# Kernel optimization log

Measured on AMD Instinct MI355X. Metric: run time of the kernel, lower is better.

The kernel has to match this reference:

```python
import jax, jax.numpy as jnp
import numpy as np

E = 64          # num_experts
TOPK = 8        # num_experts_per_tok
I = 512         # moe_intermediate_size
H = 1024        # hidden_size
G = 128         # awq group_size
T = 2048        # tokens (batch*seq)

# AWQ nibble unpack order: bit shifts [0,16,4,20,8,24,12,28] -> indices [0,4,1,5,2,6,3,7]
_AWQ_SHIFTS = jnp.array([0, 4, 1, 5, 2, 6, 3, 7], dtype=jnp.int32) * 4


def awq_dequant(qw, qz, scales, group_size=G):
    """qw: (K, N//8) int32, qz: (K//G, N//8) int32, scales: (K//G, N) float.
    Returns dense weight (K, N): (q - z) * scale with per-group zero/scale."""
    K = qw.shape[0]
    uq = ((qw[:, :, None] >> _AWQ_SHIFTS) & 0xF).reshape(K, -1)          # (K, N)
    uz = ((qz[:, :, None] >> _AWQ_SHIFTS) & 0xF).reshape(qz.shape[0], -1)  # (K//G, N)
    uz = jnp.repeat(uz, group_size, axis=0)                               # (K, N)
    sc = jnp.repeat(scales, group_size, axis=0)                           # (K, N)
    return (uq.astype(scales.dtype) - uz.astype(scales.dtype)) * sc


def setup_inputs() -> dict:
    key = jax.random.key(0)
    ks = jax.random.split(key, 8)
    imax = 2**31 - 1
    return {
        "x": jax.random.normal(ks[0], (T, H), dtype=jnp.float32),
        "gate_w": jax.random.normal(ks[1], (E, H), dtype=jnp.float32) * 0.02,
        "qweight1": jax.random.randint(ks[2], (H, (E * I) // 8), 0, imax, dtype=jnp.int32),
        "qzeros1": jax.random.randint(ks[3], (H // G, (E * I) // 8), 0, imax, dtype=jnp.int32),
        "scales1": jax.random.normal(ks[4], (H // G, E * I), dtype=jnp.float32) * 0.02,
        "qweight2": jax.random.randint(ks[5], (I, (E * H) // 8), 0, imax, dtype=jnp.int32),
        "qzeros2": jax.random.randint(ks[6], (I // G, (E * H) // 8), 0, imax, dtype=jnp.int32),
        "scales2": jax.random.normal(ks[7], (I // G, E * H), dtype=jnp.float32) * 0.02,
    }


def reference(x, gate_w, qweight1, qzeros1, scales1, qweight2, qzeros2, scales2):
    # dequant grouped expert weights
    w1 = awq_dequant(qweight1, qzeros1, scales1).T.reshape(E, I, H)   # (E, I, H)
    w2 = awq_dequant(qweight2, qzeros2, scales2).T.reshape(E, H, I)   # (E, H, I)

    # routing: softmax -> top-k -> renormalize
    logits = x @ gate_w.T                                             # (T, E)
    probs = jax.nn.softmax(logits, axis=-1)
    topv, topi = jax.lax.top_k(probs, TOPK)                           # (T, K)
    topv = topv / jnp.sum(topv, axis=-1, keepdims=True)
    cw = jnp.sum(jax.nn.one_hot(topi, E, dtype=x.dtype) * topv[..., None], axis=1)  # (T, E)

    # experts: out = sum_e cw[t,e] * silu(x @ w1[e].T) @ w2[e].T
    h = jax.nn.silu(jnp.einsum('th,eih->tei', x, w1))                 # (T, E, I)
    h = h * cw[:, :, None]                                            # fold combine weights
    out = jnp.einsum('tei,ehi->th', h, w2)                            # (T, H)
    return out
```

## Files before the change

kernel.cpp:

```cpp
#include <hip/hip_runtime.h>
#include <hip/hip_bf16.h>

#define T_TOK 2048
#define HID   1024
#define EXP   64
#define TOPK  8
#define IMED  512
#define N1 (EXP * IMED)
#define C1 (N1 / 8)
#define N2 (EXP * HID)
#define C2 (N2 / 8)

typedef _Float16 h16x2 __attribute__((ext_vector_type(2)));
typedef _Float16 h16x8 __attribute__((ext_vector_type(8)));
typedef float f32x4 __attribute__((ext_vector_type(4)));
typedef unsigned short ushortx4 __attribute__((ext_vector_type(4)));
typedef unsigned short ushortx8 __attribute__((ext_vector_type(8)));

__constant__ int kShifts[8] = {0, 16, 4, 20, 8, 24, 12, 28};

__device__ __forceinline__ void async16(const void* g, void* l) {
  __builtin_amdgcn_global_load_lds((const __attribute__((address_space(1))) void*)g,
                                   (__attribute__((address_space(3))) void*)l, 16, 0, 0);
}

__device__ __forceinline__ unsigned short f2h(float f) {
  return __builtin_bit_cast(unsigned short, (_Float16)f);
}
__device__ __forceinline__ float h2f(unsigned short b) {
  return (float)__builtin_bit_cast(_Float16, b);
}

__device__ __forceinline__ h16x8 unpack8h(unsigned q, h16x2 sh2, h16x2 zh2) {
  union { unsigned u[4]; h16x8 v; } out;
#pragma unroll
  for (int j = 0; j < 4; ++j) {
    const unsigned m = ((q >> (4 * j)) & 0x000F000Fu) | 0x64006400u;
    h16x2 d = __builtin_bit_cast(h16x2, m) - zh2;
    d = d * sh2;
    out.u[j] = __builtin_bit_cast(unsigned, d);
  }
  return out.v;
}

__global__ __launch_bounds__(256) void routing_kernel(
    const float* __restrict__ x, const float* __restrict__ gate_w,
    int* __restrict__ counts, int* __restrict__ tok_list,
    int* __restrict__ hslot_list, float* __restrict__ cw_list,
    unsigned short* __restrict__ xh) {
  const int t = blockIdx.x;
  const int tid = threadIdx.x;
  __shared__ float xs[HID];
  __shared__ float part[64][4];

  float4 v = reinterpret_cast<const float4*>(x + (size_t)t * HID)[tid];
  reinterpret_cast<float4*>(xs)[tid] = v;
  ushortx4 o;
  o[0] = f2h(v.x); o[1] = f2h(v.y); o[2] = f2h(v.z); o[3] = f2h(v.w);
  *reinterpret_cast<ushortx4*>(xh + (size_t)t * HID + tid * 4) = o;
  __syncthreads();

  const int e = tid >> 2, seg = tid & 3;
  const float4* gp = reinterpret_cast<const float4*>(gate_w + (size_t)e * HID);
  const float4* xp = reinterpret_cast<const float4*>(xs);
  float acc = 0.f;
#pragma unroll 8
  for (int i = 0; i < 64; ++i) {
    float4 a = xp[i * 4 + seg];
    float4 b = gp[i * 4 + seg];
    acc = fmaf(a.x, b.x, acc);
    acc = fmaf(a.y, b.y, acc);
    acc = fmaf(a.z, b.z, acc);
    acc = fmaf(a.w, b.w, acc);
  }
  part[e][seg] = acc;
  __syncthreads();

  if (tid < 64) {
    float4 p = reinterpret_cast<const float4*>(part)[tid];
    float lg = (p.x + p.y) + (p.z + p.w);

    float m = lg;
    for (int off = 32; off; off >>= 1) m = fmaxf(m, __shfl_xor(m, off));
    float pe = expf(lg - m);
    float s = pe;
    for (int off = 32; off; off >>= 1) s += __shfl_xor(s, off);
    float prob = pe / s;

    float pcur = prob;
    float myv = 0.f;
    int myi = -1;
    float tsum = 0.f;
    for (int k = 0; k < TOPK; ++k) {
      float vv = pcur;
      int idx = tid;
      for (int off = 32; off; off >>= 1) {
        float ov = __shfl_xor(vv, off);
        int oi = __shfl_xor(idx, off);
        if (ov > vv || (ov == vv && oi < idx)) { vv = ov; idx = oi; }
      }
      tsum += vv;
      if (tid == k) { myv = vv; myi = idx; }
      if (tid == idx) pcur = -1.f;
    }

    if (tid < TOPK) {
      float cw = myv / tsum;
      int ex = myi;
      int slot = atomicAdd(&counts[ex], 1);
      tok_list[ex * T_TOK + slot] = t;
      hslot_list[ex * T_TOK + slot] = t * TOPK + tid;
      cw_list[ex * T_TOK + slot] = cw;
    }
  }
}

__global__ __launch_bounds__(256) void repack_kernel(
    const int* __restrict__ qw, unsigned* __restrict__ qk, int K, int C) {
  const int pp = blockIdx.y;
  const int t = pp >> 2, fq = pp & 3;
  const int c2 = blockIdx.x * 512 + threadIdx.x * 2;
  const int nblk = c2 >> 1;
  unsigned o0[16], o1[16];
#pragma unroll
  for (int i = 0; i < 16; ++i) { o0[i] = 0u; o1[i] = 0u; }
  const int k0a = t * 64 + fq * 8;
  const int k0b = t * 64 + (fq + 4) * 8;
#pragma unroll
  for (int r = 0; r < 8; ++r) {
    const int2 va = *reinterpret_cast<const int2*>(qw + (size_t)(k0a + r) * C + c2);
    const int2 vb = *reinterpret_cast<const int2*>(qw + (size_t)(k0b + r) * C + c2);
    const int outsh = (r & 1) * 16 + (r >> 1) * 4;
    const unsigned qa[2] = {(unsigned)va.x, (unsigned)va.y};
    const unsigned qb[2] = {(unsigned)vb.x, (unsigned)vb.y};
#pragma unroll
    for (int ci = 0; ci < 2; ++ci) {
#pragma unroll
      for (int j = 0; j < 8; ++j) {
        const int sh = kShifts[j];
        o0[ci * 8 + j] |= ((qa[ci] >> sh) & 0xFu) << outsh;
        o1[ci * 8 + j] |= ((qb[ci] >> sh) & 0xFu) << outsh;
      }
    }
  }
  unsigned* dst = qk + (size_t)nblk * 2 * K + t * 128 + fq * 32;
#pragma unroll
  for (int idx = 0; idx < 16; ++idx)
    *reinterpret_cast<uint2*>(dst + idx * 2) = make_uint2(o0[idx], o1[idx]);
}

__global__ __launch_bounds__(256) void mfma_gemm1(
    const unsigned short* __restrict__ xh, const unsigned* __restrict__ qk1,
    const int* __restrict__ qz1, const float* __restrict__ sc1,
    const int* __restrict__ counts, const int* __restrict__ tok_list,
    const int* __restrict__ hslot_list, const float* __restrict__ cw_list,
    unsigned short* __restrict__ h_buf) {
  const int e = blockIdx.z;
  const int n_e = counts[e];
  const int t0 = blockIdx.y * 64;
  if (t0 >= n_e) return;
  const int ntile = blockIdx.x;
  const int tid = threadIdx.x;
  const int wave = tid >> 6, lane = tid & 63;
  const int fr = lane & 15, fq = lane >> 4;

  __shared__ unsigned short As[2][64 * 64];

  const int arow = tid >> 3;
  const int acb = ((tid & 7) ^ ((tid >> 3) & 7)) * 16;
  const int ta0 = tok_list[e * T_TOK + min(t0 + arow, n_e - 1)];
  const int ta1 = tok_list[e * T_TOK + min(t0 + 32 + arow, n_e - 1)];
  const char* ga0 = (const char*)(xh + (size_t)ta0 * HID) + acb;
  const char* ga1 = (const char*)(xh + (size_t)ta1 * HID) + acb;

  auto stage = [&](int b) {
    char* l = (char*)&As[b][0] + wave * 1024;
    async16(ga0, l);
    async16(ga1, l + 4096);
    ga0 += 128; ga1 += 128;
  };

  const int nbase = e * IMED + ntile * 64 + wave * 16;
  const unsigned* bp = qk1 + (size_t)(nbase >> 4) * (2 * HID) + fq * 32 + fr * 2;
  const int col = nbase + fr;
  const int shz = ((fr >> 1) & 3) * 4 + (fr & 1) * 16;

  f32x4 acc[4];
#pragma unroll
  for (int i = 0; i < 4; ++i) acc[i] = (f32x4){0.f, 0.f, 0.f, 0.f};

  stage(0);
  uint2 qcur = *reinterpret_cast<const uint2*>(bp);
  float s_cur = sc1[col];
  unsigned zd_cur = (unsigned)qz1[col >> 3];
  int p = 0;
#pragma unroll 1
  for (int g = 0; g < HID / 128; ++g) {
    const unsigned shb = (unsigned)f2h(s_cur);
    const h16x2 sh2 = __builtin_bit_cast(h16x2, shb | (shb << 16));
    const unsigned zb = 0x6400u | ((zd_cur >> shz) & 15u);
    const h16x2 zh2 = __builtin_bit_cast(h16x2, zb | (zb << 16));
    float s_nxt = 0.f; unsigned zd_nxt = 0u;
#pragma unroll
    for (int hh = 0; hh < 2; ++hh) {
      const int t = g * 2 + hh;
      __syncthreads();
      if (t + 1 < HID / 64) stage(p ^ 1);
      uint2 qnext = make_uint2(0u, 0u);
      if (t + 1 < HID / 64) qnext = *reinterpret_cast<const uint2*>(bp + (t + 1) * 128);
      if (hh == 1 && g + 1 < HID / 128) {
        s_nxt = sc1[(size_t)(g + 1) * N1 + col];
        zd_nxt = (unsigned)qz1[(size_t)(g + 1) * C1 + (col >> 3)];
      }
      const h16x8 b0 = unpack8h(qcur.x, sh2, zh2);
      const h16x8 b1 = unpack8h(qcur.y, sh2, zh2);
#pragma unroll
      for (int kk = 0; kk < 2; ++kk) {
        const h16x8 bb = kk ? b1 : b0;
#pragma unroll
        for (int i = 0; i < 4; ++i) {
          const int row = i * 16 + fr;
          const h16x8 a = *reinterpret_cast<const h16x8*>(
              &As[p][row * 64 + (((kk * 4 + fq) ^ (fr & 7)) * 8)]);
          acc[i] = __builtin_amdgcn_mfma_f32_16x16x32_f16(a, bb, acc[i], 0, 0, 0);
        }
      }
      qcur = qnext; p ^= 1;
    }
    s_cur = s_nxt; zd_cur = zd_nxt;
  }

#pragma unroll
  for (int i = 0; i < 4; ++i) {
#pragma unroll
    for (int r = 0; r < 4; ++r) {
      const int grow = t0 + i * 16 + fq * 4 + r;
      if (grow < n_e) {
        const float cw = cw_list[e * T_TOK + grow];
        const int hs = hslot_list[e * T_TOK + grow];
        const float v = acc[i][r];
        h_buf[(size_t)hs * IMED + ntile * 64 + wave * 16 + fr] =
            f2h((v / (1.f + expf(-v))) * cw);
      }
    }
  }
}

__global__ __launch_bounds__(256) void mfma_gemm2(
    const unsigned short* __restrict__ h_buf, const unsigned* __restrict__ qk2,
    const int* __restrict__ qz2, const float* __restrict__ sc2,
    const int* __restrict__ counts, const int* __restrict__ hslot_list,
    unsigned short* __restrict__ p_buf) {
  const int e = blockIdx.z;
  const int n_e = counts[e];
  const int t0 = blockIdx.y * 64;
  if (t0 >= n_e) return;
  const int ntile = blockIdx.x;
  const int tid = threadIdx.x;
  const int wave = tid >> 6, lane = tid & 63;
  const int fr = lane & 15, fq = lane >> 4;

  __shared__ unsigned short As[2][64 * 64];

  const int arow = tid >> 3;
  const int acb = ((tid & 7) ^ ((tid >> 3) & 7)) * 16;
  const int ha0 = hslot_list[e * T_TOK + min(t0 + arow, n_e - 1)];
  const int ha1 = hslot_list[e * T_TOK + min(t0 + 32 + arow, n_e - 1)];
  const char* ga0 = (const char*)(h_buf + (size_t)ha0 * IMED) + acb;
  const char* ga1 = (const char*)(h_buf + (size_t)ha1 * IMED) + acb;

  auto stage = [&](int b) {
    char* l = (char*)&As[b][0] + wave * 1024;
    async16(ga0, l);
    async16(ga1, l + 4096);
    ga0 += 128; ga1 += 128;
  };

  const int nbase = e * HID + ntile * 64 + wave * 16;
  const unsigned* bp = qk2 + (size_t)(nbase >> 4) * (2 * IMED) + fq * 32 + fr * 2;
  const int col = nbase + fr;
  const int shz = ((fr >> 1) & 3) * 4 + (fr & 1) * 16;

  f32x4 acc[4];
#pragma unroll
  for (int i = 0; i < 4; ++i) acc[i] = (f32x4){0.f, 0.f, 0.f, 0.f};

  stage(0);
  uint2 qcur = *reinterpret_cast<const uint2*>(bp);
  float s_cur = sc2[col];
  unsigned zd_cur = (unsigned)qz2[col >> 3];
  int p = 0;
#pragma unroll 1
  for (int g = 0; g < IMED / 128; ++g) {
    const unsigned shb = (unsigned)f2h(s_cur);
    const h16x2 sh2 = __builtin_bit_cast(h16x2, shb | (shb << 16));
    const unsigned zb = 0x6400u | ((zd_cur >> shz) & 15u);
    const h16x2 zh2 = __builtin_bit_cast(h16x2, zb | (zb << 16));
    float s_nxt = 0.f; unsigned zd_nxt = 0u;
#pragma unroll
    for (int hh = 0; hh < 2; ++hh) {
      const int t = g * 2 + hh;
      __syncthreads();
      if (t + 1 < IMED / 64) stage(p ^ 1);
      uint2 qnext = make_uint2(0u, 0u);
      if (t + 1 < IMED / 64) qnext = *reinterpret_cast<const uint2*>(bp + (t + 1) * 128);
      if (hh == 1 && g + 1 < IMED / 128) {
        s_nxt = sc2[(size_t)(g + 1) * N2 + col];
        zd_nxt = (unsigned)qz2[(size_t)(g + 1) * C2 + (col >> 3)];
      }
      const h16x8 b0 = unpack8h(qcur.x, sh2, zh2);
      const h16x8 b1 = unpack8h(qcur.y, sh2, zh2);
#pragma unroll
      for (int kk = 0; kk < 2; ++kk) {
        const h16x8 bb = kk ? b1 : b0;
#pragma unroll
        for (int i = 0; i < 4; ++i) {
          const int row = i * 16 + fr;
          const h16x8 a = *reinterpret_cast<const h16x8*>(
              &As[p][row * 64 + (((kk * 4 + fq) ^ (fr & 7)) * 8)]);
          acc[i] = __builtin_amdgcn_mfma_f32_16x16x32_f16(a, bb, acc[i], 0, 0, 0);
        }
      }
      qcur = qnext; p ^= 1;
    }
    s_cur = s_nxt; zd_cur = zd_nxt;
  }

#pragma unroll
  for (int i = 0; i < 4; ++i) {
#pragma unroll
    for (int r = 0; r < 4; ++r) {
      const int grow = t0 + i * 16 + fq * 4 + r;
      if (grow < n_e) {
        const int hs = hslot_list[e * T_TOK + grow];
        p_buf[(size_t)hs * HID + ntile * 64 + wave * 16 + fr] = f2h(acc[i][r]);
      }
    }
  }
}

__global__ __launch_bounds__(256) void reduce_kernel(const unsigned short* __restrict__ p_buf,
                                                     float* __restrict__ out) {
  const int idx = blockIdx.x * 256 + threadIdx.x;
  const int t = idx >> 7;
  const int c0 = (idx & 127) * 8;
  float s[8] = {0.f, 0.f, 0.f, 0.f, 0.f, 0.f, 0.f, 0.f};
#pragma unroll
  for (int k = 0; k < TOPK; ++k) {
    ushortx8 v = *reinterpret_cast<const ushortx8*>(p_buf + ((size_t)t * TOPK + k) * HID + c0);
#pragma unroll
    for (int j = 0; j < 8; ++j) s[j] += h2f(v[j]);
  }
  float* dst = out + (size_t)t * HID + c0;
  *reinterpret_cast<float4*>(dst) = make_float4(s[0], s[1], s[2], s[3]);
  *reinterpret_cast<float4*>(dst + 4) = make_float4(s[4], s[5], s[6], s[7]);
}

extern "C" void kernel_launch(void* const* d_in, const int* in_sizes, int n_in,
                              void* d_out, int out_size, void* d_ws, size_t ws_size,
                              hipStream_t stream) {
  const float* x      = (const float*)d_in[0];
  const float* gate_w = (const float*)d_in[1];
  const int*   qw1    = (const int*)d_in[2];
  const int*   qz1    = (const int*)d_in[3];
  const float* sc1    = (const float*)d_in[4];
  const int*   qw2    = (const int*)d_in[5];
  const int*   qz2    = (const int*)d_in[6];
  const float* sc2    = (const float*)d_in[7];
  float* out = (float*)d_out;

  char* ws = (char*)d_ws;
  int* counts           = (int*)(ws);
  int* tok_list         = (int*)(ws + 256);
  int* hslot_list       = (int*)(ws + 524544);
  float* cw_list        = (float*)(ws + 1048832);
  unsigned short* h_buf = (unsigned short*)(ws + 1573120);
  unsigned short* xh    = (unsigned short*)(ws + 18350336);
  unsigned* qk1         = (unsigned*)(ws + 22544640);
  unsigned* qk2         = (unsigned*)(ws + 39321856);
  unsigned short* p_buf = (unsigned short*)(ws + 56099072);

  hipMemsetAsync(counts, 0, 256, stream);

  routing_kernel<<<T_TOK, 256, 0, stream>>>(x, gate_w, counts, tok_list, hslot_list, cw_list, xh);
  repack_kernel<<<dim3(C1 / 512, HID / 16), 256, 0, stream>>>(qw1, qk1, HID, C1);
  repack_kernel<<<dim3(C2 / 512, IMED / 16), 256, 0, stream>>>(qw2, qk2, IMED, C2);

  mfma_gemm1<<<dim3(IMED / 64, T_TOK / 64, EXP), 256, 0, stream>>>(
      xh, qk1, qz1, sc1, counts, tok_list, hslot_list, cw_list, h_buf);
  mfma_gemm2<<<dim3(HID / 64, T_TOK / 64, EXP), 256, 0, stream>>>(
      h_buf, qk2, qz2, sc2, counts, hslot_list, p_buf);
  reduce_kernel<<<(T_TOK * HID / 8) / 256, 256, 0, stream>>>(p_buf, out);
}
```

Before: 265.5 us.

## Split routing into cast, tiled split-K logits GEMM, and per-wave top-k kernels

Replaces the one-block-per-token routing kernel with three kernels: a flat fp32-to-fp16 cast of x, a tiled 64x64 logits GEMM that splits K into 8 partial sums and uses XOR-swizzled shared memory, and a top-k kernel that processes one token per wave. The old kernel read the full gate matrix from cache for every token and had only 64 of 256 threads doing softmax and top-k. In exchange it adds two kernel launches and a partial-logits buffer in workspace, and the summation order of the logits changes, which could alter top-k ties.

```diff
diff --git a/kernel.cpp b/kernel.cpp
--- a/kernel.cpp
+++ b/kernel.cpp
@@ -43,75 +43,112 @@
   return out.v;
 }
 
-__global__ __launch_bounds__(256) void routing_kernel(
-    const float* __restrict__ x, const float* __restrict__ gate_w,
-    int* __restrict__ counts, int* __restrict__ tok_list,
-    int* __restrict__ hslot_list, float* __restrict__ cw_list,
-    unsigned short* __restrict__ xh) {
-  const int t = blockIdx.x;
-  const int tid = threadIdx.x;
-  __shared__ float xs[HID];
-  __shared__ float part[64][4];
-
-  float4 v = reinterpret_cast<const float4*>(x + (size_t)t * HID)[tid];
-  reinterpret_cast<float4*>(xs)[tid] = v;
+__global__ __launch_bounds__(256) void cast_x_kernel(const float* __restrict__ x,
+                                                     unsigned short* __restrict__ xh) {
+  const int i = (blockIdx.x * 256 + threadIdx.x) * 4;
+  float4 v = *reinterpret_cast<const float4*>(x + i);
   ushortx4 o;
   o[0] = f2h(v.x); o[1] = f2h(v.y); o[2] = f2h(v.z); o[3] = f2h(v.w);
-  *reinterpret_cast<ushortx4*>(xh + (size_t)t * HID + tid * 4) = o;
+  *reinterpret_cast<ushortx4*>(xh + i) = o;
+}
+
+__global__ __launch_bounds__(256) void logits_f32_kernel(
+    const float* __restrict__ x, const float* __restrict__ gate_w,
+    float* __restrict__ partial) {
+  const int t0 = blockIdx.x * 64;
+  const int k0 = blockIdx.y * 128;
+  const int tid = threadIdx.x;
+
+  __shared__ float xs[64][128];
+  __shared__ float gs[64][128];
+
+  const int lrow = tid >> 5;
+  const int cblk = tid & 31;
+#pragma unroll
+  for (int r = 0; r < 8; ++r) {
+    const int row = r * 8 + lrow;
+    const int sc = (cblk ^ ((row >> 2) & 7)) * 4;
+    float4 xv = *reinterpret_cast<const float4*>(x + (size_t)(t0 + row) * HID + k0 + cblk * 4);
+    float4 gv = *reinterpret_cast<const float4*>(gate_w + (size_t)row * HID + k0 + cblk * 4);
+    *reinterpret_cast<float4*>(&xs[row][sc]) = xv;
+    *reinterpret_cast<float4*>(&gs[row][sc]) = gv;
+  }
   __syncthreads();
 
-  const int e = tid >> 2, seg = tid & 3;
-  const float4* gp = reinterpret_cast<const float4*>(gate_w + (size_t)e * HID);
-  const float4* xp = reinterpret_cast<const float4*>(xs);
-  float acc = 0.f;
+  const int tg = (tid >> 4) * 4;
+  const int eg = (tid & 15) * 4;
+  const int xsw = (tid >> 4) & 7;
+  const int gsw = tid & 7;
+  float acc[4][4] = {{0.f}};
 #pragma unroll 8
-  for (int i = 0; i < 64; ++i) {
-    float4 a = xp[i * 4 + seg];
-    float4 b = gp[i * 4 + seg];
-    acc = fmaf(a.x, b.x, acc);
-    acc = fmaf(a.y, b.y, acc);
-    acc = fmaf(a.z, b.z, acc);
-    acc = fmaf(a.w, b.w, acc);
-  }
-  part[e][seg] = acc;
-  __syncthreads();
-
-  if (tid < 64) {
-    float4 p = reinterpret_cast<const float4*>(part)[tid];
-    float lg = (p.x + p.y) + (p.z + p.w);
-
-    float m = lg;
-    for (int off = 32; off; off >>= 1) m = fmaxf(m, __shfl_xor(m, off));
-    float pe = expf(lg - m);
-    float s = pe;
-    for (int off = 32; off; off >>= 1) s += __shfl_xor(s, off);
-    float prob = pe / s;
-
-    float pcur = prob;
-    float myv = 0.f;
-    int myi = -1;
-    float tsum = 0.f;
-    for (int k = 0; k < TOPK; ++k) {
-      float vv = pcur;
-      int idx = tid;
-      for (int off = 32; off; off >>= 1) {
-        float ov = __shfl_xor(vv, off);
-        int oi = __shfl_xor(idx, off);
-        if (ov > vv || (ov == vv && oi < idx)) { vv = ov; idx = oi; }
-      }
-      tsum += vv;
-      if (tid == k) { myv = vv; myi = idx; }
-      if (tid == idx) pcur = -1.f;
-    }
-
-    if (tid < TOPK) {
-      float cw = myv / tsum;
-      int ex = myi;
-      int slot = atomicAdd(&counts[ex], 1);
-      tok_list[ex * T_TOK + slot] = t;
-      hslot_list[ex * T_TOK + slot] = t * TOPK + tid;
-      cw_list[ex * T_TOK + slot] = cw;
-    }
+  for (int k = 0; k < 128; k += 4) {
+    const int c = k >> 2;
+    float4 a[4], b[4];
+#pragma unroll
+    for (int i = 0; i < 4; ++i)
+      a[i] = *reinterpret_cast<const float4*>(&xs[tg + i][(c ^ xsw) * 4]);
+#pragma unroll
+    for (int j = 0; j < 4; ++j)
+      b[j] = *reinterpret_cast<const float4*>(&gs[eg + j][(c ^ gsw) * 4]);
+#pragma unroll
+    for (int i = 0; i < 4; ++i)
+#pragma unroll
+      for (int j = 0; j < 4; ++j) {
+        acc[i][j] = fmaf(a[i].x, b[j].x, acc[i][j]);
+        acc[i][j] = fmaf(a[i].y, b[j].y, acc[i][j]);
+        acc[i][j] = fmaf(a[i].z, b[j].z, acc[i][j]);
+        acc[i][j] = fmaf(a[i].w, b[j].w, acc[i][j]);
+      }
+  }
+  float* dst = partial + ((size_t)blockIdx.y * T_TOK + t0) * EXP;
+#pragma unroll
+  for (int i = 0; i < 4; ++i)
+    *reinterpret_cast<float4*>(dst + (tg + i) * EXP + eg) =
+        make_float4(acc[i][0], acc[i][1], acc[i][2], acc[i][3]);
+}
+
+__global__ __launch_bounds__(256) void topk_kernel(
+    const float* __restrict__ partial, int* __restrict__ counts,
+    int* __restrict__ tok_list, int* __restrict__ hslot_list,
+    float* __restrict__ cw_list) {
+  const int wave = threadIdx.x >> 6, lane = threadIdx.x & 63;
+  const int t = blockIdx.x * 4 + wave;
+  float lg = 0.f;
+#pragma unroll
+  for (int s = 0; s < 8; ++s)
+    lg += partial[((size_t)s * T_TOK + t) * EXP + lane];
+
+  float m = lg;
+  for (int off = 32; off; off >>= 1) m = fmaxf(m, __shfl_xor(m, off));
+  float pe = expf(lg - m);
+  float s = pe;
+  for (int off = 32; off; off >>= 1) s += __shfl_xor(s, off);
+  float prob = pe / s;
+
+  float pcur = prob;
+  float myv = 0.f;
+  int myi = -1;
+  float tsum = 0.f;
+  for (int k = 0; k < TOPK; ++k) {
+    float vv = pcur;
+    int idx = lane;
+    for (int off = 32; off; off >>= 1) {
+      float ov = __shfl_xor(vv, off);
+      int oi = __shfl_xor(idx, off);
+      if (ov > vv || (ov == vv && oi < idx)) { vv = ov; idx = oi; }
+    }
+    tsum += vv;
+    if (lane == k) { myv = vv; myi = idx; }
+    if (lane == idx) pcur = -1.f;
+  }
+
+  if (lane < TOPK) {
+    const float cw = myv / tsum;
+    const int ex = myi;
+    const int slot = atomicAdd(&counts[ex], 1);
+    tok_list[ex * T_TOK + slot] = t;
+    hslot_list[ex * T_TOK + slot] = t * TOPK + lane;
+    cw_list[ex * T_TOK + slot] = cw;
   }
 }
 
@@ -379,10 +416,13 @@
   unsigned* qk1         = (unsigned*)(ws + 22544640);
   unsigned* qk2         = (unsigned*)(ws + 39321856);
   unsigned short* p_buf = (unsigned short*)(ws + 56099072);
+  float* partial        = (float*)(ws + 89653504);
 
   hipMemsetAsync(counts, 0, 256, stream);
 
-  routing_kernel<<<T_TOK, 256, 0, stream>>>(x, gate_w, counts, tok_list, hslot_list, cw_list, xh);
+  cast_x_kernel<<<(T_TOK * HID / 4) / 256, 256, 0, stream>>>(x, xh);
+  logits_f32_kernel<<<dim3(T_TOK / 64, HID / 128), 256, 0, stream>>>(x, gate_w, partial);
+  topk_kernel<<<T_TOK / 4, 256, 0, stream>>>(partial, counts, tok_list, hslot_list, cw_list);
   repack_kernel<<<dim3(C1 / 512, HID / 16), 256, 0, stream>>>(qw1, qk1, HID, C1);
   repack_kernel<<<dim3(C2 / 512, IMED / 16), 256, 0, stream>>>(qw2, qk2, IMED, C2);
 
```

New measurement: 254.5 us. 1.04x faster.
